# Optimization experiments

Hardware: AMD Instinct MI355X
Metric: run time of the kernel (lower is better)

The kernel has to match this reference:

```python
import jax, jax.numpy as jnp
import numpy as np

N = 50000          # total nodes
N_USER = 40000     # main (user) nodes
E = 400000         # edges per node kind
K = 3              # node kinds (separate graphs)
H = 4              # attention heads
F_IN = 128         # n_units[0]
F_OUT = 64         # n_units[1]
NB_CLASSES = 40
SLOPE = 0.2        # leaky relu negative slope


def setup_inputs() -> dict:
    key = jax.random.key(0)
    ks = jax.random.split(key, 12)
    h = jax.random.normal(ks[0], (N, F_IN), dtype=jnp.float32)
    edge_index = jax.random.randint(ks[1], (K, 2, E), 0, N, dtype=jnp.int32)
    # per-kind SpGATLayer params (bias=False)
    w = jax.random.normal(ks[2], (K, H, F_IN, F_OUT), dtype=jnp.float32) * 0.1
    a_src = jax.random.normal(ks[3], (K, H, F_OUT), dtype=jnp.float32) * 0.1
    a_trg = jax.random.normal(ks[4], (K, H, F_OUT), dtype=jnp.float32) * 0.1
    # AdditiveAttention: w1 (d=F_IN -> d2=F_OUT), w2 (d1=F_OUT -> d2=F_OUT), m (d2 -> 1)
    w1 = jax.random.normal(ks[5], (F_IN, F_OUT), dtype=jnp.float32) * 0.1
    w2 = jax.random.normal(ks[6], (F_OUT, F_OUT), dtype=jnp.float32) * 0.1
    m = jax.random.normal(ks[7], (F_OUT,), dtype=jnp.float32) * 0.1
    # final fc: in = F_OUT*(K+1)
    fc_w = jax.random.normal(ks[8], (F_OUT * (K + 1), NB_CLASSES), dtype=jnp.float32) * 0.1
    fc_b = jnp.zeros((NB_CLASSES,), dtype=jnp.float32)
    return {"h": h, "edge_index": edge_index, "w": w, "a_src": a_src,
            "a_trg": a_trg, "w1": w1, "w2": w2, "m": m,
            "fc_w": fc_w, "fc_b": fc_b}


def _spgat_kind(h, src, trg, wk, ask, atk):
    # h: [N, F_IN], wk: [H, F_IN, F_OUT], ask/atk: [H, F_OUT]
    hp = jnp.einsum('nd,hdf->nhf', h, wk)               # [N, H, F_OUT]
    s = jnp.einsum('nhf,hf->nh', hp, ask)               # [N, H]
    t = jnp.einsum('nhf,hf->nh', hp, atk)               # [N, H]
    e = s[src] + t[trg]                                 # [E, H]
    e = jnp.where(e >= 0, e, SLOPE * e)                 # leaky relu
    e = e - jnp.max(e)                                  # global max shift (as in source)
    exp_e = jnp.exp(e)
    denom = jax.ops.segment_sum(exp_e, trg, num_segments=N)  # [N, H]
    alpha = exp_e / (denom[trg] + 1e-16)                # [E, H]
    msg = hp[src] * alpha[:, :, None]                   # [E, H, F_OUT]
    out = jax.ops.segment_sum(msg, trg, num_segments=N) # [N, H, F_OUT]
    return out.mean(axis=1)                             # [N, F_OUT] (last layer head-mean)


def reference(h, edge_index, w, a_src, a_trg, w1, w2, m, fc_w, fc_b):
    heter = []
    for k in range(K):  # fixed small loop over node kinds
        x = _spgat_kind(h, edge_index[k, 0], edge_index[k, 1],
                        w[k], a_src[k], a_trg[k])
        heter.append(x[:N_USER])
    type_aware = jnp.stack(heter, axis=1)               # [N_USER, K, F_OUT]
    feature = h[:N_USER]                                # [N_USER, F_IN]
    q = jnp.tanh((feature @ w1)[:, None, :] + type_aware @ w2)  # [N_USER, K, F_OUT]
    scores = q @ m                                      # [N_USER, K]
    beta = jax.nn.softmax(scores, axis=-1)
    fusion = jnp.einsum('nk,nkf->nf', beta, type_aware) # [N_USER, F_OUT]
    ret = jnp.concatenate([type_aware, fusion[:, None, :]], axis=1)
    ret = ret.reshape(N_USER, -1)                       # [N_USER, F_OUT*(K+1)]
    logits = ret @ fc_w + fc_b
    return jax.nn.log_softmax(logits, axis=-1)
```

## Files before the change

### kernel.cpp

```cpp
#include <hip/hip_runtime.h>
#include <hip/hip_bf16.h>

#define NN    50000
#define NUSER 40000
#define EE    400000
#define KKIND 3
#define HHEAD 4
#define FIN   128
#define FOUT  64
#define NCLS  40

typedef __attribute__((ext_vector_type(8))) short short8;
typedef __attribute__((ext_vector_type(4))) float floatx4;

__device__ __forceinline__ float bf2f(unsigned short u) {
    unsigned int v = ((unsigned int)u) << 16;
    return __uint_as_float(v);
}
__device__ __forceinline__ unsigned short f2bf(float f) {
    unsigned int u = __float_as_uint(f);
    unsigned int r = (u + 0x7FFFu + ((u >> 16) & 1u)) >> 16;
    return (unsigned short)r;
}

#define OFF_H    0
#define OFF_W    6400000
#define OFF_ASRC 6498304
#define OFF_ATRG 6499072
#define OFF_W1   6499840
#define OFF_W2   6508032
#define OFF_M    6512128
#define OFF_FCW  6512192
#define OFF_FCB  6522432
#define CONV_TOT 6522472

__global__ __launch_bounds__(256) void detect_kernel(const unsigned short* __restrict__ hraw,
                                                     int* __restrict__ flag)
{
    __shared__ int cnt;
    if (threadIdx.x == 0) cnt = 0;
    __syncthreads();
    int local = 0;
#pragma unroll
    for (int j = 0; j < 8; j++) {
        unsigned short u = hraw[threadIdx.x * 8 + j];
        int ex = (u >> 7) & 0xFF;
        if (ex >= 0x90) local++;
    }
    atomicAdd(&cnt, local);
    __syncthreads();
    if (threadIdx.x == 0) *flag = (cnt > 100) ? 1 : 0;
}

__global__ __launch_bounds__(256) void conv_kernel(const void* __restrict__ p0, const void* __restrict__ p2,
                                                   const void* __restrict__ p3, const void* __restrict__ p4,
                                                   const void* __restrict__ p5, const void* __restrict__ p6,
                                                   const void* __restrict__ p7, const void* __restrict__ p8,
                                                   const void* __restrict__ p9,
                                                   const int* __restrict__ flagp,
                                                   unsigned short* __restrict__ dst)
{
    int tid = (blockIdx.x * 256 + threadIdx.x) * 8;
    if (tid >= CONV_TOT) return;
    const void* src; int li;
    if      (tid < OFF_W)    { src = p0; li = tid - OFF_H; }
    else if (tid < OFF_ASRC) { src = p2; li = tid - OFF_W; }
    else if (tid < OFF_ATRG) { src = p3; li = tid - OFF_ASRC; }
    else if (tid < OFF_W1)   { src = p4; li = tid - OFF_ATRG; }
    else if (tid < OFF_W2)   { src = p5; li = tid - OFF_W1; }
    else if (tid < OFF_M)    { src = p6; li = tid - OFF_W2; }
    else if (tid < OFF_FCW)  { src = p7; li = tid - OFF_M; }
    else if (tid < OFF_FCB)  { src = p8; li = tid - OFF_FCW; }
    else                     { src = p9; li = tid - OFF_FCB; }
    if (*flagp) {
        const float* fp = (const float*)src + li;
        float4 x = *(const float4*)fp;
        float4 y = *(const float4*)(fp + 4);
        uint4 o;
        o.x = (unsigned int)f2bf(x.x) | ((unsigned int)f2bf(x.y) << 16);
        o.y = (unsigned int)f2bf(x.z) | ((unsigned int)f2bf(x.w) << 16);
        o.z = (unsigned int)f2bf(y.x) | ((unsigned int)f2bf(y.y) << 16);
        o.w = (unsigned int)f2bf(y.z) | ((unsigned int)f2bf(y.w) << 16);
        *(uint4*)(dst + tid) = o;
    } else {
        *(uint4*)(dst + tid) = *(const uint4*)((const unsigned short*)src + li);
    }
}

__global__ __launch_bounds__(256) void repack_w(const unsigned short* __restrict__ w,
                                                unsigned short* __restrict__ wT)
{
    int tid = blockIdx.x * 256 + threadIdx.x;
    if (tid >= 12288) return;
    int f = tid & 63, g = (tid >> 6) & 15, h = (tid >> 10) & 3, k = tid >> 12;
    const unsigned short* src = w + (size_t)(k * 4 + h) * 8192 + f;
    unsigned short* dst = wT + (size_t)tid * 8;
#pragma unroll
    for (int j = 0; j < 8; j++) dst[j] = src[(size_t)(g * 8 + j) * 64];
}

__global__ __launch_bounds__(256) void repack_small(const unsigned short* __restrict__ w1,
                                                    const unsigned short* __restrict__ w2,
                                                    const unsigned short* __restrict__ fcw,
                                                    unsigned short* __restrict__ w1T,
                                                    unsigned short* __restrict__ w2T,
                                                    unsigned short* __restrict__ fcwT)
{
    int tid = blockIdx.x * 256 + threadIdx.x;
    if (tid < 1024) {
        int c = tid & 63, g = tid >> 6;
#pragma unroll
        for (int j = 0; j < 8; j++) w1T[(size_t)(g * 64 + c) * 8 + j] = w1[(size_t)(g * 8 + j) * 64 + c];
    } else if (tid < 1536) {
        int t = tid - 1024; int c = t & 63, g = t >> 6;
#pragma unroll
        for (int j = 0; j < 8; j++) w2T[(size_t)(g * 64 + c) * 8 + j] = w2[(size_t)(g * 8 + j) * 64 + c];
    } else if (tid < 3072) {
        int t = tid - 1536; int c = t % 48, g = t / 48;
#pragma unroll
        for (int j = 0; j < 8; j++)
            fcwT[(size_t)(g * 48 + c) * 8 + j] = (c < NCLS) ? fcw[(size_t)(g * 8 + j) * NCLS + c] : (unsigned short)0;
    }
}

__global__ __launch_bounds__(256) void repack_ast(const unsigned short* __restrict__ asrc_all,
                                                  const unsigned short* __restrict__ atrg_all,
                                                  unsigned short* __restrict__ bst)
{
    int tid = blockIdx.x * 256 + threadIdx.x;
    if (tid >= 1536) return;
    int c = tid & 15, g = (tid >> 4) & 31, k = tid >> 9;
    const unsigned short* ask = asrc_all + k * 256;
    const unsigned short* atk = atrg_all + k * 256;
    unsigned short* dst = bst + (size_t)tid * 8;
#pragma unroll
    for (int j = 0; j < 8; j++) {
        int kd = g * 8 + j;
        int f = kd >> 2, hh = kd & 3;
        unsigned short v = 0;
        if (c < 4)      { if (hh == c)     v = ask[c * 64 + f]; }
        else if (c < 8) { if (hh == c - 4) v = atk[(c - 4) * 64 + f]; }
        dst[j] = v;
    }
}

__global__ __launch_bounds__(256) void hist3(const int* __restrict__ ei,
                                             unsigned int* __restrict__ cnt,
                                             unsigned int* __restrict__ rank)
{
    int k = blockIdx.y;
    const int* trg = ei + (size_t)k * 2 * EE + EE;
    unsigned int* ck = cnt + (size_t)k * NUSER;
    unsigned int* rk = rank + (size_t)k * EE;
    int e0 = blockIdx.x * 1024 + threadIdx.x;
    int t[4];
#pragma unroll
    for (int j = 0; j < 4; j++) {
        int e = e0 + j * 256;
        t[j] = (e < EE) ? trg[e] : NUSER;
    }
    unsigned int r[4];
#pragma unroll
    for (int j = 0; j < 4; j++)
        r[j] = (t[j] < NUSER) ? atomicAdd(&ck[t[j]], 1u) : 0u;
#pragma unroll
    for (int j = 0; j < 4; j++) {
        int e = e0 + j * 256;
        if (e < EE && t[j] < NUSER) rk[e] = r[j];
    }
}

#define SCB 20
__global__ __launch_bounds__(256) void scanA(const unsigned int* __restrict__ cnt,
                                             unsigned int* __restrict__ partials)
{
    int k = blockIdx.y, b = blockIdx.x;
    const unsigned int* c = cnt + (size_t)k * NUSER;
    int base = b * 2048 + threadIdx.x * 8;
    unsigned int s = 0;
#pragma unroll
    for (int j = 0; j < 8; j++) { int idx = base + j; if (idx < NUSER) s += c[idx]; }
#pragma unroll
    for (int off = 1; off < 64; off <<= 1) s += __shfl_xor(s, off, 64);
    __shared__ unsigned int wsum[4];
    int lane = threadIdx.x & 63, wid = threadIdx.x >> 6;
    if (lane == 0) wsum[wid] = s;
    __syncthreads();
    if (threadIdx.x == 0) partials[k * SCB + b] = wsum[0] + wsum[1] + wsum[2] + wsum[3];
}

__global__ __launch_bounds__(256) void scanB(unsigned int* __restrict__ partials,
                                             unsigned int* __restrict__ rowptr)
{
    int wid = threadIdx.x >> 6, lane = threadIdx.x & 63;
    if (wid >= KKIND) return;
    unsigned int v = (lane < SCB) ? partials[wid * SCB + lane] : 0u;
    unsigned int inc = v;
#pragma unroll
    for (int off = 1; off < 32; off <<= 1) {
        unsigned int u = __shfl_up(inc, off, 64);
        if (lane >= off) inc += u;
    }
    if (lane < SCB) partials[wid * SCB + lane] = inc - v;
    if (lane == SCB - 1) rowptr[(size_t)wid * (NUSER + 1) + NUSER] = inc;
}

__global__ __launch_bounds__(256) void scanC(const unsigned int* __restrict__ cnt,
                                             const unsigned int* __restrict__ partials,
                                             unsigned int* __restrict__ rowptr)
{
    int k = blockIdx.y, b = blockIdx.x;
    const unsigned int* c = cnt + (size_t)k * NUSER;
    unsigned int* rp = rowptr + (size_t)k * (NUSER + 1);
    int lane = threadIdx.x & 63, wid = threadIdx.x >> 6;
    int base = b * 2048 + threadIdx.x * 8;
    unsigned int vals[8]; unsigned int s = 0;
#pragma unroll
    for (int j = 0; j < 8; j++) { int idx = base + j; vals[j] = (idx < NUSER) ? c[idx] : 0u; s += vals[j]; }
    unsigned int inc = s;
#pragma unroll
    for (int off = 1; off < 64; off <<= 1) {
        unsigned int u = __shfl_up(inc, off, 64);
        if (lane >= off) inc += u;
    }
    __shared__ unsigned int wsum[4];
    if (lane == 63) wsum[wid] = inc;
    __syncthreads();
    unsigned int woff = 0;
    for (int i = 0; i < wid; i++) woff += wsum[i];
    unsigned int run = partials[k * SCB + b] + woff + (inc - s);
#pragma unroll
    for (int j = 0; j < 8; j++) {
        int idx = base + j;
        if (idx < NUSER) { rp[idx] = run; run += vals[j]; }
    }
}

__global__ __launch_bounds__(256) void scatter3(const int* __restrict__ ei,
                                                const unsigned int* __restrict__ rowptr,
                                                const unsigned int* __restrict__ rank,
                                                int* __restrict__ srcl)
{
    int k = blockIdx.y;
    const int* srcA = ei + (size_t)k * 2 * EE;
    const int* trg = srcA + EE;
    const unsigned int* rp = rowptr + (size_t)k * (NUSER + 1);
    const unsigned int* rk = rank + (size_t)k * EE;
    int* sl = srcl + (size_t)k * EE;
    int e0 = blockIdx.x * 1024 + threadIdx.x;
    int t[4], s[4]; unsigned int r[4];
#pragma unroll
    for (int j = 0; j < 4; j++) {
        int e = e0 + j * 256;
        t[j] = (e < EE) ? trg[e] : NUSER;
        s[j] = (e < EE) ? srcA[e] : 0;
        r[j] = (e < EE && t[j] < NUSER) ? rk[e] : 0u;
    }
    unsigned int base[4];
#pragma unroll
    for (int j = 0; j < 4; j++) base[j] = (t[j] < NUSER) ? rp[t[j]] : 0u;
#pragma unroll
    for (int j = 0; j < 4; j++) {
        int e = e0 + j * 256;
        if (e < EE && t[j] < NUSER) sl[base[j] + r[j]] = s[j];
    }
}

__global__ __launch_bounds__(256) void hp_gemm2(const unsigned short* __restrict__ h,
                                                const unsigned short* __restrict__ wTall,
                                                unsigned short* __restrict__ hp2,
                                                long long hp2_stride, int kbeg)
{
    int k = kbeg + blockIdx.y;
    const unsigned short* wTk = wTall + (size_t)k * 32768;
    unsigned short* hp2k = hp2 + (size_t)blockIdx.y * hp2_stride;

    int q = threadIdx.x >> 6;
    int lane = threadIdx.x & 63;
    int m0 = blockIdx.x * 16;
    int mi = lane & 15, quad = lane >> 4;

    short8 a[4];
    const unsigned short* hrow = h + (size_t)(m0 + mi) * FIN + quad * 8;
#pragma unroll
    for (int kk = 0; kk < 4; kk++) a[kk] = *(const short8*)(hrow + kk * 32);

    int fc = q * 16 + mi;
    floatx4 acc4[4];
#pragma unroll
    for (int hh = 0; hh < 4; hh++) {
        floatx4 acc = {0.f, 0.f, 0.f, 0.f};
#pragma unroll
        for (int kk = 0; kk < 4; kk++) {
            short8 b = *(const short8*)(wTk + (size_t)((hh * 16 + kk * 4 + quad) * 64 + fc) * 8);
            acc = __builtin_amdgcn_mfma_f32_16x16x32_bf16(a[kk], b, acc, 0, 0, 0);
        }
        acc4[hh] = acc;
    }
#pragma unroll
    for (int reg = 0; reg < 4; reg++) {
        ushort4 pk;
        pk.x = f2bf(acc4[0][reg]); pk.y = f2bf(acc4[1][reg]);
        pk.z = f2bf(acc4[2][reg]); pk.w = f2bf(acc4[3][reg]);
        int row = m0 + quad * 4 + reg;
        *(ushort4*)(hp2k + (size_t)row * 256 + fc * 4) = pk;
    }
}

__global__ __launch_bounds__(256) void st_gemm(const unsigned short* __restrict__ hp2,
                                               long long hp2_stride,
                                               const unsigned short* __restrict__ bst,
                                               float* __restrict__ sb, float* __restrict__ tb,
                                               int kbeg)
{
    int kq = blockIdx.y, k = kbeg + kq;
    const unsigned short* hp2k = hp2 + (size_t)kq * hp2_stride;
    const unsigned short* bk = bst + (size_t)k * 4096;
    float* sbk = sb + (size_t)k * NN * 4;
    float* tbk = tb + (size_t)k * NN * 4;

    int wave = threadIdx.x >> 6;
    int lane = threadIdx.x & 63;
    int m0 = (blockIdx.x * 4 + wave) * 16;
    if (m0 >= NN) return;
    int mi = lane & 15, quad = lane >> 4;

    floatx4 acc = {0.f, 0.f, 0.f, 0.f};
#pragma unroll
    for (int kk = 0; kk < 8; kk++) {
        short8 a = *(const short8*)(hp2k + (size_t)(m0 + mi) * 256 + kk * 32 + quad * 8);
        short8 b = *(const short8*)(bk + (size_t)((kk * 4 + quad) * 16 + mi) * 8);
        acc = __builtin_amdgcn_mfma_f32_16x16x32_bf16(a, b, acc, 0, 0, 0);
    }
    if (mi < 8) {
#pragma unroll
        for (int reg = 0; reg < 4; reg++) {
            int n = m0 + quad * 4 + reg;
            if (mi < 4) sbk[n * 4 + mi] = acc[reg];
            else        tbk[n * 4 + (mi - 4)] = acc[reg];
        }
    }
}

__global__ __launch_bounds__(256) void passB_multi(const unsigned int* __restrict__ rowptr_all,
                                                   const int* __restrict__ srcl_all,
                                                   const float* __restrict__ sb,
                                                   const float* __restrict__ tb,
                                                   const unsigned short* __restrict__ hp2,
                                                   long long hp2_stride,
                                                   unsigned short* __restrict__ ret, int kbeg)
{
    __shared__ int    lds_src[4][64];
    __shared__ float4 lds_ew[4][64];
    int kq = blockIdx.y, k = kbeg + kq;
    const unsigned int* rowptr = rowptr_all + (size_t)k * (NUSER + 1);
    const int* srcl = srcl_all + (size_t)k * EE;
    const float* sbk = sb + (size_t)k * NN * 4;
    const float* tbk = tb + (size_t)k * NN * 4;
    const unsigned short* hp2k = hp2 + (size_t)kq * hp2_stride;

    int wid = threadIdx.x >> 6;
    int n = __builtin_amdgcn_readfirstlane(blockIdx.x * 4 + wid);
    int f = threadIdx.x & 63;
    unsigned int beg = rowptr[n], end = rowptr[n + 1];
    float4 t4 = *(const float4*)(tbk + (size_t)n * 4);
    float num0 = 0.f, num1 = 0.f, num2 = 0.f, num3 = 0.f;
    float den0 = 0.f, den1 = 0.f, den2 = 0.f, den3 = 0.f;

    for (unsigned int p0 = beg; p0 < end; p0 += 64) {
        unsigned int cnt = end - p0; if (cnt > 64) cnt = 64;
        int s = 0;
        float4 e = {0.f, 0.f, 0.f, 0.f};
        if ((unsigned int)f < cnt) {
            s = srcl[p0 + f];
            float4 sv = *(const float4*)(sbk + (size_t)s * 4);
            float v0 = sv.x + t4.x, v1 = sv.y + t4.y, v2 = sv.z + t4.z, v3 = sv.w + t4.w;
            v0 = (v0 >= 0.f) ? v0 : 0.2f * v0;  v1 = (v1 >= 0.f) ? v1 : 0.2f * v1;
            v2 = (v2 >= 0.f) ? v2 : 0.2f * v2;  v3 = (v3 >= 0.f) ? v3 : 0.2f * v3;
            e.x = __expf(v0); e.y = __expf(v1); e.z = __expf(v2); e.w = __expf(v3);
        }
        lds_src[wid][f] = s;
        lds_ew[wid][f] = e;
        float d0 = e.x, d1 = e.y, d2 = e.z, d3 = e.w;
#pragma unroll
        for (int off = 1; off < 64; off <<= 1) {
            d0 += __shfl_xor(d0, off, 64); d1 += __shfl_xor(d1, off, 64);
            d2 += __shfl_xor(d2, off, 64); d3 += __shfl_xor(d3, off, 64);
        }
        den0 += d0; den1 += d1; den2 += d2; den3 += d3;
        unsigned int jmax = (cnt + 7u) & ~7u;
        for (unsigned int j = 0; j < jmax; j += 8) {
            int ss[8]; float4 ee[8];
#pragma unroll
            for (int u = 0; u < 8; u++) { ss[u] = lds_src[wid][j + u]; ee[u] = lds_ew[wid][j + u]; }
            ushort4 hv[8];
#pragma unroll
            for (int u = 0; u < 8; u++) hv[u] = *(const ushort4*)(hp2k + (size_t)ss[u] * 256 + f * 4);
#pragma unroll
            for (int u = 0; u < 8; u++) {
                num0 += ee[u].x * bf2f(hv[u].x); num1 += ee[u].y * bf2f(hv[u].y);
                num2 += ee[u].z * bf2f(hv[u].z); num3 += ee[u].w * bf2f(hv[u].w);
            }
        }
    }
    float r = 0.25f * (num0 / (den0 + 1e-16f) + num1 / (den1 + 1e-16f)
                     + num2 / (den2 + 1e-16f) + num3 / (den3 + 1e-16f));
    ret[(size_t)n * 256 + k * 64 + f] = f2bf(r);
}

__global__ __launch_bounds__(256) void qscore2f(const unsigned short* __restrict__ h,
                                                const unsigned short* __restrict__ w1T,
                                                const unsigned short* __restrict__ retA,
                                                const unsigned short* __restrict__ w2T,
                                                const unsigned short* __restrict__ mvec,
                                                unsigned short* __restrict__ ret, int M)
{
    int wave = (blockIdx.x * 256 + threadIdx.x) >> 6;
    int lane = threadIdx.x & 63;
    int m0 = wave * 16;
    if (m0 >= M) return;
    int mi = lane & 15, quad = lane >> 4;

    floatx4 fw[4];
#pragma unroll
    for (int nt = 0; nt < 4; nt++) fw[nt] = (floatx4){0.f, 0.f, 0.f, 0.f};
#pragma unroll
    for (int kk = 0; kk < 4; kk++) {
        short8 a = *(const short8*)(h + (size_t)(m0 + mi) * FIN + kk * 32 + quad * 8);
#pragma unroll
        for (int nt = 0; nt < 4; nt++) {
            short8 b = *(const short8*)(w1T + (size_t)((kk * 4 + quad) * 64 + nt * 16 + mi) * 8);
            fw[nt] = __builtin_amdgcn_mfma_f32_16x16x32_bf16(a, b, fw[nt], 0, 0, 0);
        }
    }

    float pk[3][4];
    short8 afr[3][2];
    for (int k = 0; k < KKIND; k++) {
        floatx4 acc[4];
#pragma unroll
        for (int nt = 0; nt < 4; nt++) acc[nt] = (floatx4){0.f, 0.f, 0.f, 0.f};
#pragma unroll
        for (int kk = 0; kk < 2; kk++) {
            short8 a = *(const short8*)(retA + (size_t)(m0 + mi) * 256 + k * 64 + kk * 32 + quad * 8);
            afr[k][kk] = a;
#pragma unroll
            for (int nt = 0; nt < 4; nt++) {
                short8 b = *(const short8*)(w2T + (size_t)((kk * 4 + quad) * 64 + nt * 16 + mi) * 8);
                acc[nt] = __builtin_amdgcn_mfma_f32_16x16x32_bf16(a, b, acc[nt], 0, 0, 0);
            }
        }
        float part[4] = {0.f, 0.f, 0.f, 0.f};
#pragma unroll
        for (int nt = 0; nt < 4; nt++) {
            int col = nt * 16 + mi;
            float mval = bf2f(mvec[col]);
#pragma unroll
            for (int reg = 0; reg < 4; reg++) {
                float x = acc[nt][reg] + fw[nt][reg];
                float q = 1.f - 2.f / (1.f + __expf(2.f * x));
                part[reg] += q * mval;
            }
        }
#pragma unroll
        for (int off = 1; off < 16; off <<= 1)
#pragma unroll
            for (int reg = 0; reg < 4; reg++) part[reg] += __shfl_xor(part[reg], off, 64);
#pragma unroll
        for (int reg = 0; reg < 4; reg++) pk[k][reg] = part[reg];
    }

    int rsel = mi & 3;
    float sv0 = (rsel == 0) ? pk[0][0] : (rsel == 1) ? pk[0][1] : (rsel == 2) ? pk[0][2] : pk[0][3];
    float sv1 = (rsel == 0) ? pk[1][0] : (rsel == 1) ? pk[1][1] : (rsel == 2) ? pk[1][2] : pk[1][3];
    float sv2 = (rsel == 0) ? pk[2][0] : (rsel == 1) ? pk[2][1] : (rsel == 2) ? pk[2][2] : pk[2][3];
    int srcLane = ((mi >> 2) << 4) | mi;
    float s0 = __shfl(sv0, srcLane, 64);
    float s1 = __shfl(sv1, srcLane, 64);
    float s2 = __shfl(sv2, srcLane, 64);
    float mx = fmaxf(s0, fmaxf(s1, s2));
    float e0 = __expf(s0 - mx), e1 = __expf(s1 - mx), e2 = __expf(s2 - mx);
    float inv = 1.f / (e0 + e1 + e2);
    float w0 = e0 * inv, w1 = e1 * inv, w2 = e2 * inv;

#pragma unroll
    for (int kk = 0; kk < 2; kk++) {
        unsigned short pkd[8];
#pragma unroll
        for (int j = 0; j < 8; j++) {
            float fu = w0 * bf2f((unsigned short)afr[0][kk][j])
                     + w1 * bf2f((unsigned short)afr[1][kk][j])
                     + w2 * bf2f((unsigned short)afr[2][kk][j]);
            pkd[j] = f2bf(fu);
        }
        *(ushort4*)(ret + (size_t)(m0 + mi) * 256 + 192 + kk * 32 + quad * 8) =
            *(ushort4*)&pkd[0];
        *(ushort4*)(ret + (size_t)(m0 + mi) * 256 + 192 + kk * 32 + quad * 8 + 4) =
            *(ushort4*)&pkd[4];
    }
}

__global__ __launch_bounds__(256) void fc_lsm(const unsigned short* __restrict__ A,
                                              const unsigned short* __restrict__ fcwT,
                                              const unsigned short* __restrict__ bias,
                                              const int* __restrict__ flagp,
                                              void* __restrict__ out, int M)
{
    int wave = (blockIdx.x * 256 + threadIdx.x) >> 6;
    int lane = threadIdx.x & 63;
    int m0 = wave * 16;
    if (m0 >= M) return;
    int mi = lane & 15, quad = lane >> 4;
    floatx4 acc[3];
#pragma unroll
    for (int nt = 0; nt < 3; nt++) acc[nt] = (floatx4){0.f, 0.f, 0.f, 0.f};
#pragma unroll
    for (int kk = 0; kk < 8; kk++) {
        short8 a = *(const short8*)(A + (size_t)(m0 + mi) * 256 + kk * 32 + quad * 8);
#pragma unroll
        for (int nt = 0; nt < 3; nt++) {
            short8 b = *(const short8*)(fcwT + (size_t)((kk * 4 + quad) * 48 + nt * 16 + mi) * 8);
            acc[nt] = __builtin_amdgcn_mfma_f32_16x16x32_bf16(a, b, acc[nt], 0, 0, 0);
        }
    }
    int fl = *flagp;
    float bv[3]; bool ok[3];
#pragma unroll
    for (int nt = 0; nt < 3; nt++) {
        int col = nt * 16 + mi;
        ok[nt] = (col < NCLS);
        bv[nt] = ok[nt] ? bf2f(bias[col]) : 0.f;
    }
#pragma unroll
    for (int reg = 0; reg < 4; reg++) {
        float v[3];
#pragma unroll
        for (int nt = 0; nt < 3; nt++)
            v[nt] = ok[nt] ? (acc[nt][reg] + bv[nt]) : -3.4e38f;
        float mx = fmaxf(fmaxf(v[0], v[1]), v[2]);
#pragma unroll
        for (int off = 1; off < 16; off <<= 1) mx = fmaxf(mx, __shfl_xor(mx, off, 64));
        float s = 0.f;
#pragma unroll
        for (int nt = 0; nt < 3; nt++) s += ok[nt] ? __expf(v[nt] - mx) : 0.f;
#pragma unroll
        for (int off = 1; off < 16; off <<= 1) s += __shfl_xor(s, off, 64);
        float lse = mx + __logf(s);
        int row = m0 + quad * 4 + reg;
#pragma unroll
        for (int nt = 0; nt < 3; nt++) {
            int col = nt * 16 + mi;
            if (col < NCLS) {
                float ls = v[nt] - lse;
                size_t idx = (size_t)row * NCLS + col;
                if (fl) ((float*)out)[idx] = ls;
                else    ((unsigned short*)out)[idx] = f2bf(ls);
            }
        }
    }
}

extern "C" void kernel_launch(void* const* d_in, const int* in_sizes, int n_in,
                              void* d_out, int out_size, void* d_ws, size_t ws_size,
                              hipStream_t stream)
{
    (void)in_sizes; (void)n_in; (void)out_size;
    const int* ei = (const int*)d_in[1];

    char* ws = (char*)d_ws;
    unsigned short* conv = (unsigned short*)ws;
    unsigned short* hc   = conv + OFF_H;
    unsigned short* wc   = conv + OFF_W;
    unsigned short* asrc = conv + OFF_ASRC;
    unsigned short* atrg = conv + OFF_ATRG;
    unsigned short* w1c  = conv + OFF_W1;
    unsigned short* w2c  = conv + OFF_W2;
    unsigned short* mc   = conv + OFF_M;
    unsigned short* fcwc = conv + OFF_FCW;
    unsigned short* fcbc = conv + OFF_FCB;
    int* flag             = (int*)(ws + 13044944);
    unsigned short* wT    = (unsigned short*)(ws + 13045248);
    unsigned short* w1T   = (unsigned short*)(ws + 13241856);
    unsigned short* w2T   = (unsigned short*)(ws + 13258240);
    unsigned short* fcwT  = (unsigned short*)(ws + 13266432);
    unsigned short* bst   = (unsigned short*)(ws + 13291008);
    unsigned int* partials= (unsigned int*)(ws + 13315584);
    unsigned int* cnt     = (unsigned int*)(ws + 13315840);
    unsigned int* rowptr  = (unsigned int*)(ws + 13795840);
    int* srcl             = (int*)(ws + 14276096);
    unsigned int* rank    = (unsigned int*)(ws + 19076096);
    float* sbuf           = (float*)(ws + 23876096);
    float* tbuf           = (float*)(ws + 26276096);
    unsigned short* ret   = (unsigned short*)(ws + 28676096);
    unsigned short* hp2   = (unsigned short*)(ws + 49156096);

    const size_t NEED_BIG = 49156096ull + 3ull * NN * 256 * 2;
    int big = (ws_size >= NEED_BIG) ? 1 : 0;

    detect_kernel<<<1, 256, 0, stream>>>((const unsigned short*)d_in[0], flag);
    conv_kernel<<<(CONV_TOT / 8 + 255) / 256, 256, 0, stream>>>(
        d_in[0], d_in[2], d_in[3], d_in[4], d_in[5], d_in[6], d_in[7], d_in[8], d_in[9],
        flag, conv);

    repack_w<<<48, 256, 0, stream>>>(wc, wT);
    repack_small<<<12, 256, 0, stream>>>(w1c, w2c, fcwc, w1T, w2T, fcwT);
    repack_ast<<<6, 256, 0, stream>>>(asrc, atrg, bst);

    hipMemsetAsync(cnt, 0, (size_t)KKIND * NUSER * 4, stream);
    hist3<<<dim3((EE + 1023) / 1024, 3), 256, 0, stream>>>(ei, cnt, rank);
    scanA<<<dim3(SCB, 3), 256, 0, stream>>>(cnt, partials);
    scanB<<<1, 256, 0, stream>>>(partials, rowptr);
    scanC<<<dim3(SCB, 3), 256, 0, stream>>>(cnt, partials, rowptr);
    scatter3<<<dim3((EE + 1023) / 1024, 3), 256, 0, stream>>>(ei, rowptr, rank, srcl);

    if (big) {
        long long stride = (long long)NN * 256;
        hp_gemm2<<<dim3(NN / 16, 3), 256, 0, stream>>>(hc, wT, hp2, stride, 0);
        st_gemm<<<dim3((NN / 16 + 3) / 4, 3), 256, 0, stream>>>(hp2, stride, bst, sbuf, tbuf, 0);
        for (int k = 0; k < KKIND; k++)
            passB_multi<<<dim3(NUSER / 4, 1), 256, 0, stream>>>(rowptr, srcl, sbuf, tbuf,
                                                                hp2 + (size_t)k * stride, 0, ret, k);
    } else {
        for (int k = 0; k < KKIND; k++) {
            hp_gemm2<<<dim3(NN / 16, 1), 256, 0, stream>>>(hc, wT, hp2, 0, k);
            st_gemm<<<dim3((NN / 16 + 3) / 4, 1), 256, 0, stream>>>(hp2, 0, bst, sbuf, tbuf, k);
            passB_multi<<<dim3(NUSER / 4, 1), 256, 0, stream>>>(rowptr, srcl, sbuf, tbuf,
                                                                hp2, 0, ret, k);
        }
    }

    qscore2f<<<625, 256, 0, stream>>>(hc, w1T, ret, w2T, mc, ret, NUSER);
    fc_lsm<<<625, 256, 0, stream>>>(ret, fcwT, fcbc, flag, d_out, NUSER);
}
```

Baseline: 340.4 us.

## Fuse attention-fusion scoring with final FC/log-softmax and loop kinds in hp GEMM

Merges the qscore kernel and the fc_lsm kernel into one. The fused fusion vector and the per-kind features stay in registers and feed the FC MFMA directly, so the fusion columns are no longer written to and re-read from global memory and one launch goes away. The hp GEMM now loops over the three kinds inside one block and reuses the loaded h fragments, instead of using a grid y-dimension per kind. This cuts redundant h loads but reduces grid parallelism and raises register pressure in the fused kernel.

```diff
diff --git a/kernel.cpp b/kernel.cpp
--- a/kernel.cpp
+++ b/kernel.cpp
@@ -266,15 +266,11 @@
     }
 }
 
-__global__ __launch_bounds__(256) void hp_gemm2(const unsigned short* __restrict__ h,
+__global__ __launch_bounds__(256) void hp_gemm3(const unsigned short* __restrict__ h,
                                                 const unsigned short* __restrict__ wTall,
                                                 unsigned short* __restrict__ hp2,
-                                                long long hp2_stride, int kbeg)
-{
-    int k = kbeg + blockIdx.y;
-    const unsigned short* wTk = wTall + (size_t)k * 32768;
-    unsigned short* hp2k = hp2 + (size_t)blockIdx.y * hp2_stride;
-
+                                                long long hp2_stride, int kbeg, int kcnt)
+{
     int q = threadIdx.x >> 6;
     int lane = threadIdx.x & 63;
     int m0 = blockIdx.x * 16;
@@ -286,24 +282,28 @@
     for (int kk = 0; kk < 4; kk++) a[kk] = *(const short8*)(hrow + kk * 32);
 
     int fc = q * 16 + mi;
-    floatx4 acc4[4];
-#pragma unroll
-    for (int hh = 0; hh < 4; hh++) {
-        floatx4 acc = {0.f, 0.f, 0.f, 0.f};
-#pragma unroll
-        for (int kk = 0; kk < 4; kk++) {
-            short8 b = *(const short8*)(wTk + (size_t)((hh * 16 + kk * 4 + quad) * 64 + fc) * 8);
-            acc = __builtin_amdgcn_mfma_f32_16x16x32_bf16(a[kk], b, acc, 0, 0, 0);
-        }
-        acc4[hh] = acc;
-    }
-#pragma unroll
-    for (int reg = 0; reg < 4; reg++) {
-        ushort4 pk;
-        pk.x = f2bf(acc4[0][reg]); pk.y = f2bf(acc4[1][reg]);
-        pk.z = f2bf(acc4[2][reg]); pk.w = f2bf(acc4[3][reg]);
-        int row = m0 + quad * 4 + reg;
-        *(ushort4*)(hp2k + (size_t)row * 256 + fc * 4) = pk;
+    for (int kq = 0; kq < kcnt; kq++) {
+        const unsigned short* wTk = wTall + (size_t)(kbeg + kq) * 32768;
+        unsigned short* hp2k = hp2 + (size_t)kq * hp2_stride;
+        floatx4 acc4[4];
+#pragma unroll
+        for (int hh = 0; hh < 4; hh++) {
+            floatx4 acc = {0.f, 0.f, 0.f, 0.f};
+#pragma unroll
+            for (int kk = 0; kk < 4; kk++) {
+                short8 b = *(const short8*)(wTk + (size_t)((hh * 16 + kk * 4 + quad) * 64 + fc) * 8);
+                acc = __builtin_amdgcn_mfma_f32_16x16x32_bf16(a[kk], b, acc, 0, 0, 0);
+            }
+            acc4[hh] = acc;
+        }
+#pragma unroll
+        for (int reg = 0; reg < 4; reg++) {
+            ushort4 pk;
+            pk.x = f2bf(acc4[0][reg]); pk.y = f2bf(acc4[1][reg]);
+            pk.z = f2bf(acc4[2][reg]); pk.w = f2bf(acc4[3][reg]);
+            int row = m0 + quad * 4 + reg;
+            *(ushort4*)(hp2k + (size_t)row * 256 + fc * 4) = pk;
+        }
     }
 }
 
@@ -408,12 +408,15 @@
     ret[(size_t)n * 256 + k * 64 + f] = f2bf(r);
 }
 
-__global__ __launch_bounds__(256) void qscore2f(const unsigned short* __restrict__ h,
-                                                const unsigned short* __restrict__ w1T,
-                                                const unsigned short* __restrict__ retA,
-                                                const unsigned short* __restrict__ w2T,
-                                                const unsigned short* __restrict__ mvec,
-                                                unsigned short* __restrict__ ret, int M)
+__global__ __launch_bounds__(256) void qscore_fc(const unsigned short* __restrict__ h,
+                                                 const unsigned short* __restrict__ w1T,
+                                                 const unsigned short* __restrict__ retA,
+                                                 const unsigned short* __restrict__ w2T,
+                                                 const unsigned short* __restrict__ mvec,
+                                                 const unsigned short* __restrict__ fcwT,
+                                                 const unsigned short* __restrict__ bias,
+                                                 const int* __restrict__ flagp,
+                                                 void* __restrict__ out, int M)
 {
     int wave = (blockIdx.x * 256 + threadIdx.x) >> 6;
     int lane = threadIdx.x & 63;
@@ -478,48 +481,31 @@
     float s0 = __shfl(sv0, srcLane, 64);
     float s1 = __shfl(sv1, srcLane, 64);
     float s2 = __shfl(sv2, srcLane, 64);
-    float mx = fmaxf(s0, fmaxf(s1, s2));
-    float e0 = __expf(s0 - mx), e1 = __expf(s1 - mx), e2 = __expf(s2 - mx);
+    float mx0 = fmaxf(s0, fmaxf(s1, s2));
+    float e0 = __expf(s0 - mx0), e1 = __expf(s1 - mx0), e2 = __expf(s2 - mx0);
     float inv = 1.f / (e0 + e1 + e2);
     float w0 = e0 * inv, w1 = e1 * inv, w2 = e2 * inv;
 
-#pragma unroll
-    for (int kk = 0; kk < 2; kk++) {
-        unsigned short pkd[8];
+    short8 ffr[2];
+#pragma unroll
+    for (int kk = 0; kk < 2; kk++)
 #pragma unroll
         for (int j = 0; j < 8; j++) {
             float fu = w0 * bf2f((unsigned short)afr[0][kk][j])
                      + w1 * bf2f((unsigned short)afr[1][kk][j])
                      + w2 * bf2f((unsigned short)afr[2][kk][j]);
-            pkd[j] = f2bf(fu);
-        }
-        *(ushort4*)(ret + (size_t)(m0 + mi) * 256 + 192 + kk * 32 + quad * 8) =
-            *(ushort4*)&pkd[0];
-        *(ushort4*)(ret + (size_t)(m0 + mi) * 256 + 192 + kk * 32 + quad * 8 + 4) =
-            *(ushort4*)&pkd[4];
-    }
-}
-
-__global__ __launch_bounds__(256) void fc_lsm(const unsigned short* __restrict__ A,
-                                              const unsigned short* __restrict__ fcwT,
-                                              const unsigned short* __restrict__ bias,
-                                              const int* __restrict__ flagp,
-                                              void* __restrict__ out, int M)
-{
-    int wave = (blockIdx.x * 256 + threadIdx.x) >> 6;
-    int lane = threadIdx.x & 63;
-    int m0 = wave * 16;
-    if (m0 >= M) return;
-    int mi = lane & 15, quad = lane >> 4;
+            ffr[kk][j] = (short)f2bf(fu);
+        }
+
     floatx4 acc[3];
 #pragma unroll
     for (int nt = 0; nt < 3; nt++) acc[nt] = (floatx4){0.f, 0.f, 0.f, 0.f};
 #pragma unroll
-    for (int kk = 0; kk < 8; kk++) {
-        short8 a = *(const short8*)(A + (size_t)(m0 + mi) * 256 + kk * 32 + quad * 8);
+    for (int kp = 0; kp < 8; kp++) {
+        short8 a = (kp < 6) ? afr[kp >> 1][kp & 1] : ffr[kp - 6];
 #pragma unroll
         for (int nt = 0; nt < 3; nt++) {
-            short8 b = *(const short8*)(fcwT + (size_t)((kk * 4 + quad) * 48 + nt * 16 + mi) * 8);
+            short8 b = *(const short8*)(fcwT + (size_t)((kp * 4 + quad) * 48 + nt * 16 + mi) * 8);
             acc[nt] = __builtin_amdgcn_mfma_f32_16x16x32_bf16(a, b, acc[nt], 0, 0, 0);
         }
     }
@@ -615,20 +601,19 @@
 
     if (big) {
         long long stride = (long long)NN * 256;
-        hp_gemm2<<<dim3(NN / 16, 3), 256, 0, stream>>>(hc, wT, hp2, stride, 0);
+        hp_gemm3<<<dim3(NN / 16, 1), 256, 0, stream>>>(hc, wT, hp2, stride, 0, 3);
         st_gemm<<<dim3((NN / 16 + 3) / 4, 3), 256, 0, stream>>>(hp2, stride, bst, sbuf, tbuf, 0);
         for (int k = 0; k < KKIND; k++)
             passB_multi<<<dim3(NUSER / 4, 1), 256, 0, stream>>>(rowptr, srcl, sbuf, tbuf,
                                                                 hp2 + (size_t)k * stride, 0, ret, k);
     } else {
         for (int k = 0; k < KKIND; k++) {
-            hp_gemm2<<<dim3(NN / 16, 1), 256, 0, stream>>>(hc, wT, hp2, 0, k);
+            hp_gemm3<<<dim3(NN / 16, 1), 256, 0, stream>>>(hc, wT, hp2, 0, k, 1);
             st_gemm<<<dim3((NN / 16 + 3) / 4, 1), 256, 0, stream>>>(hp2, 0, bst, sbuf, tbuf, k);
             passB_multi<<<dim3(NUSER / 4, 1), 256, 0, stream>>>(rowptr, srcl, sbuf, tbuf,
                                                                 hp2, 0, ret, k);
         }
     }
 
-    qscore2f<<<625, 256, 0, stream>>>(hc, w1T, ret, w2T, mc, ret, NUSER);
-    fc_lsm<<<625, 256, 0, stream>>>(ret, fcwT, fcbc, flag, d_out, NUSER);
-}
+    qscore_fc<<<625, 256, 0, stream>>>(hc, w1T, ret, w2T, mc, fcwT, fcbc, flag, d_out, NUSER);
+}
```

After: 330.5 us. 1.03x faster.
